# Performance work log

Hardware: AMD Instinct MI355X
Metric: run time of the kernel (lower is better)

## Reference

```python
import jax, jax.numpy as jnp
import numpy as np

N = 1_000_000   # active voxels
CIN = 32
COUT = 64
K = 9           # 3x3 kernel offsets (rulebook size)
EPS = 1e-5


def setup_inputs() -> dict:
    key = jax.random.key(0)
    ks = jax.random.split(key, 6)
    x = jax.random.normal(ks[0], (N, CIN), dtype=jnp.float32)
    # rulebook: neighbor index per (voxel, kernel offset); stride=1 so same coord set
    nbr = jax.random.randint(ks[1], (N, K), 0, N, dtype=jnp.int32)
    W1 = jax.random.normal(ks[2], (K, CIN, COUT), dtype=jnp.float32) * (1.0 / np.sqrt(K * CIN))
    W2 = jax.random.normal(ks[3], (K, COUT, COUT), dtype=jnp.float32) * (1.0 / np.sqrt(K * COUT))
    Wd = jax.random.normal(ks[4], (CIN, COUT), dtype=jnp.float32) * (1.0 / np.sqrt(CIN))
    g1 = jnp.ones((COUT,), jnp.float32); b1 = jnp.zeros((COUT,), jnp.float32)
    g2 = jnp.ones((COUT,), jnp.float32); b2 = jnp.zeros((COUT,), jnp.float32)
    gd = jnp.ones((COUT,), jnp.float32); bd = jnp.zeros((COUT,), jnp.float32)
    return {"x": x, "W1": W1, "g1": g1, "b1": b1, "W2": W2, "g2": g2, "b2": b2,
            "Wd": Wd, "gd": gd, "bd": bd, "nbr": nbr}


def _sparse_conv(x, nbr, W):
    # gather-GEMM-scatter; loop over the fixed K=9 kernel offsets to avoid
    # materializing the full [N, K, Cin] gathered tensor
    out = jnp.zeros((x.shape[0], W.shape[-1]), dtype=x.dtype)
    for k in range(W.shape[0]):
        out = out + jnp.take(x, nbr[:, k], axis=0) @ W[k]
    return out


def _bn(x, gamma, beta):
    # BatchNorm1d over the voxel dimension (training-mode batch statistics)
    mu = jnp.mean(x, axis=0)
    var = jnp.var(x, axis=0)
    return gamma * (x - mu) * jax.lax.rsqrt(var + EPS) + beta


def reference(x, W1, g1, b1, W2, g2, b2, Wd, gd, bd, nbr):
    # downsample branch (1x1 conv -> BN, no relu) since in_ch != out_ch
    identity = _bn(x @ Wd, gd, bd)
    # conv1: SparseConv3x3 -> BN -> ReLU
    out = jax.nn.relu(_bn(_sparse_conv(x, nbr, W1), g1, b1))
    # conv2: SparseConv3x3 -> BN (no relu)
    out = _bn(_sparse_conv(out, nbr, W2), g2, b2)
    # residual add + final ReLU
    return jax.nn.relu(out + identity)
```

## Files before the change

kernel.cpp:

```cpp
#include <hip/hip_runtime.h>
#include <hip/hip_bf16.h>

#define NV 1000000
#define CI 32
#define CO 64
#define KK 9
#define NG (NV / 16)
#define EPSV 1e-5f

typedef __bf16 bf16x8 __attribute__((ext_vector_type(8)));
typedef __bf16 bf16x4 __attribute__((ext_vector_type(4)));
typedef float  f32x4  __attribute__((ext_vector_type(4)));

__device__ __forceinline__ f32x4 mfma16(bf16x8 a, bf16x8 b, f32x4 c) {
    return __builtin_amdgcn_mfma_f32_16x16x32_bf16(a, b, c, 0, 0, 0);
}

__device__ __forceinline__ float xredseg(float v) {
    v += __shfl_xor(v, 16, 64);
    v += __shfl_xor(v, 32, 64);
    return v;
}

__global__ void k_prep_w(const float* __restrict__ W1, const float* __restrict__ W2,
                         const float* __restrict__ Wd,
                         __bf16* __restrict__ W1T, __bf16* __restrict__ W2T,
                         __bf16* __restrict__ WdT) {
    int i = blockIdx.x * blockDim.x + threadIdx.x;
    const int n1 = KK * CO * CI;
    const int n2 = KK * CO * CO;
    const int nd = CO * CI;
    if (i < n1) {
        int k = i / (CO * CI), r = i % (CO * CI), co = r / CI, ci = r % CI;
        W1T[i] = (__bf16)W1[(k * CI + ci) * CO + co];
    } else if (i < n1 + n2) {
        int j = i - n1;
        int k = j / (CO * CO), r = j % (CO * CO), co = r / CO, ci = r % CO;
        W2T[j] = (__bf16)W2[(k * CO + ci) * CO + co];
    } else if (i < n1 + n2 + nd) {
        int j = i - n1 - n2;
        int co = j / CI, ci = j % CI;
        WdT[j] = (__bf16)Wd[ci * CO + co];
    }
}

__global__ void k_prep_x(const float* __restrict__ x, __bf16* __restrict__ xb) {
    int i = blockIdx.x * blockDim.x + threadIdx.x;
    const float4* px = (const float4*)x + 2 * (size_t)i;
    float4 u = px[0], v = px[1];
    bf16x8 o;
    o[0] = (__bf16)u.x; o[1] = (__bf16)u.y; o[2] = (__bf16)u.z; o[3] = (__bf16)u.w;
    o[4] = (__bf16)v.x; o[5] = (__bf16)v.y; o[6] = (__bf16)v.z; o[7] = (__bf16)v.w;
    *((bf16x8*)xb + i) = o;
}

__global__ __launch_bounds__(256, 2) void k_conv1(
    const __bf16* __restrict__ xb, const int* __restrict__ nbr,
    const __bf16* __restrict__ W1T, const __bf16* __restrict__ WdT,
    __bf16* __restrict__ y1b, float* __restrict__ stats) {
    __shared__ __align__(16) char w1smem[KK * CO * CI * 2];
    __shared__ __align__(16) char ystage[4][2048];

    const int lane = threadIdx.x & 63;
    const int w    = threadIdx.x >> 6;
    const int r    = lane & 15;
    const int seg  = lane >> 4;
    const int sseg = seg ^ ((r >> 1) & 3);

#pragma unroll
    for (int j = 0; j < 9; j++) {
        int c    = j * 256 + threadIdx.x;
        int segc = c & 3;
        int rc   = (c >> 2) & 15;
        int csrc = (c & ~3) | (segc ^ ((rc >> 1) & 3));
        const __bf16* srcp = W1T + (size_t)csrc * 8;
        __builtin_amdgcn_global_load_lds(
            (const __attribute__((address_space(1))) void*)srcp,
            (__attribute__((address_space(3))) void*)(w1smem + j * 4096 + w * 1024),
            16, 0, 0);
    }
    __syncthreads();

    bf16x8 wd[4];
#pragma unroll
    for (int t = 0; t < 4; t++)
        wd[t] = *(const bf16x8*)(WdT + (size_t)(t * 16 + r) * CI + seg * 8);

    float ps1[4] = {0.f,0.f,0.f,0.f}, pq1[4] = {0.f,0.f,0.f,0.f};
    float psd[4] = {0.f,0.f,0.f,0.f}, pqd[4] = {0.f,0.f,0.f,0.f};

    const int slot   = blockIdx.x * 4 + w;
    const int stride = gridDim.x * 4;
    const f32x4 z = {0.f, 0.f, 0.f, 0.f};

    auto loadIdx = [&](int (&idx)[KK], int tile) {
        const int* nb = nbr + (size_t)(tile * 16 + r) * KK;
#pragma unroll
        for (int k = 0; k < KK; k++) idx[k] = nb[k];
    };
    auto gather9 = [&](bf16x8 (&g)[KK], const int (&idx)[KK]) {
#pragma unroll
        for (int k = 0; k < KK; k++)
            g[k] = *(const bf16x8*)(xb + (size_t)idx[k] * CI + seg * 8);
    };
    auto loadAd = [&](int tile) {
        return *(const bf16x8*)(xb + (size_t)(tile * 16 + r) * CI + seg * 8);
    };
    auto compute = [&](int tile, const bf16x8 (&g)[KK], bf16x8 ad) {
        int w1off = 0;
        asm volatile("" : "+v"(w1off));
        const __bf16* wb = (const __bf16*)w1smem + w1off;

        f32x4 acc[4]  = {z, z, z, z};
        f32x4 accd[4] = {z, z, z, z};
#pragma unroll
        for (int t = 0; t < 4; t++) accd[t] = mfma16(ad, wd[t], accd[t]);
#pragma unroll
        for (int k = 0; k < KK; k++) {
#pragma unroll
            for (int t = 0; t < 4; t++) {
                bf16x8 b = *(const bf16x8*)(wb + k * 2048 + t * 512 + r * 32 + sseg * 8);
                acc[t] = mfma16(g[k], b, acc[t]);
            }
        }

        const int vb = tile * 16;
        char* yst = ystage[w];
#pragma unroll
        for (int t = 0; t < 4; t++) {
#pragma unroll
            for (int rr = 0; rr < 4; rr++) {
                float val = acc[t][rr];
                ps1[t] += val; pq1[t] += val * val;
                float dv = accd[t][rr];
                psd[t] += dv; pqd[t] += dv * dv;
                int row = seg * 4 + rr;
                int byte = row * 128 + ((t * 32 + 2 * r) ^ ((row & 7) << 4));
                *(__bf16*)(yst + byte) = (__bf16)val;
            }
        }
#pragma unroll
        for (int q = 0; q < 2; q++) {
            int c    = lane * 2 + q;
            int row  = c >> 3;
            int part = c & 7;
            bf16x8 v = *(const bf16x8*)(yst + row * 128 + ((part ^ (row & 7)) << 4));
            __builtin_nontemporal_store(
                v, (bf16x8*)(y1b + (size_t)vb * CO + (size_t)c * 8));
        }
    };

    int idx0[KK], idx1[KK];
    bf16x8 g0[KK], g1[KK];
    bf16x8 ad0, ad1;

    int it = slot;
    loadIdx(idx0, it);
    gather9(g0, idx0); ad0 = loadAd(it);
    int itn = it + stride;
    bool have = (itn < NG);
    if (have) loadIdx(idx1, itn);

    while (true) {
        if (have) {
            gather9(g1, idx1); ad1 = loadAd(itn);
            int it2 = itn + stride;
            if (it2 < NG) loadIdx(idx0, it2);
        }
        compute(it, g0, ad0);
        if (!have) break;
        it = itn; itn = it + stride; have = (itn < NG);

        if (have) {
            gather9(g0, idx0); ad0 = loadAd(itn);
            int it2 = itn + stride;
            if (it2 < NG) loadIdx(idx1, it2);
        }
        compute(it, g1, ad1);
        if (!have) break;
        it = itn; itn = it + stride; have = (itn < NG);
    }

#pragma unroll
    for (int t = 0; t < 4; t++) {
        ps1[t] = xredseg(ps1[t]); pq1[t] = xredseg(pq1[t]);
        psd[t] = xredseg(psd[t]); pqd[t] = xredseg(pqd[t]);
    }
    if (lane < 16) {
#pragma unroll
        for (int t = 0; t < 4; t++) {
            atomicAdd(&stats[0 * 64 + t * 16 + lane], ps1[t]);
            atomicAdd(&stats[1 * 64 + t * 16 + lane], pq1[t]);
            atomicAdd(&stats[2 * 64 + t * 16 + lane], psd[t]);
            atomicAdd(&stats[3 * 64 + t * 16 + lane], pqd[t]);
        }
    }
}

#define TILE_B (16 * KK * 128)

template <bool BF16OUT>
__global__ __launch_bounds__(128, 2) void k_conv2(
    const __bf16* __restrict__ h1b, const int* __restrict__ nbr,
    const __bf16* __restrict__ W2T, const float* __restrict__ g1,
    const float* __restrict__ b1,
    __bf16* __restrict__ y2b, float* __restrict__ y2f,
    float* __restrict__ stats) {
    __shared__ __align__(16) char smem[2][TILE_B];
    __shared__ __align__(16) char ystage2[2][1024];

    const int lane = threadIdx.x & 63;
    const int w    = threadIdx.x >> 6;
    const int r    = lane & 15;
    const int seg  = lane >> 4;
    const int p    = lane & 7;

    bf16x8 w2[KK][2][2];
#pragma unroll
    for (int k = 0; k < KK; k++)
#pragma unroll
        for (int t2 = 0; t2 < 2; t2++)
#pragma unroll
            for (int s = 0; s < 2; s++) {
                int co = w * 32 + t2 * 16 + r;
                int ci = s * 32 + seg * 8;
                w2[k][t2][s] = *(const bf16x8*)(W2T + ((size_t)(k * CO + co)) * CO + ci);
            }

    float scP[8], shP[8];
#pragma unroll
    for (int j = 0; j < 8; j++) {
        int c0 = p * 8 + j;
        float mu  = stats[c0] * (1.0f / NV);
        float var = stats[64 + c0] * (1.0f / NV) - mu * mu;
        float s   = g1[c0] * rsqrtf(var + EPSV);
        scP[j] = s; shP[j] = b1[c0] - mu * s;
    }

    int ri[9], dstoff[9];
#pragma unroll
    for (int s = 0; s < 9; s++) {
        int c = w * 576 + s * 64 + lane;
        int rIdx = c >> 3;
        int i = (rIdx * 57) >> 9;
        ri[s] = rIdx;
        dstoff[s] = rIdx * 128 + ((p ^ (i & 7)) * 16);
    }

    auto loadIdx = [&](int (&ix)[9], int tile) {
        const int* nb = nbr + (size_t)tile * (16 * KK);
#pragma unroll
        for (int s = 0; s < 9; s++) ix[s] = nb[ri[s]];
    };
    auto loadDat = [&](f32x4 (&d)[9], const int (&ix)[9]) {
#pragma unroll
        for (int s = 0; s < 9; s++)
            d[s] = *(const f32x4*)(h1b + (size_t)ix[s] * CO + p * 8);
    };
    auto xform = [&](char* tb, const f32x4 (&d)[9]) {
#pragma unroll
        for (int s = 0; s < 9; s++) {
            union { f32x4 f; bf16x8 b; } u; u.f = d[s];
            bf16x8 o;
#pragma unroll
            for (int j = 0; j < 8; j++)
                o[j] = (__bf16)fmaxf((float)u.b[j] * scP[j] + shP[j], 0.f);
            *(bf16x8*)(tb + dstoff[s]) = o;
        }
    };

    float ps[2] = {0.f, 0.f}, pq[2] = {0.f, 0.f};
    const f32x4 z = {0.f, 0.f, 0.f, 0.f};
    const int sw = r & 7;
    const int G = gridDim.x;

    int idxN[9]; f32x4 dat[9];
    int it = blockIdx.x;
    loadIdx(idxN, it);
    loadDat(dat, idxN);
    { int t1 = it + G;     loadIdx(idxN, t1 < NG ? t1 : NG - 1); }
    xform(smem[0], dat);
    loadDat(dat, idxN);
    { int t2 = it + 2 * G; loadIdx(idxN, t2 < NG ? t2 : NG - 1); }
    __syncthreads();
    int cur = 0;

    for (; it < NG; it += G) {
        const __bf16* base = (const __bf16*)smem[cur];
        f32x4 acc[2] = {z, z};
#pragma unroll
        for (int k = 0; k < KK; k++) {
            const __bf16* rp = base + (size_t)(r * KK + k) * 64;
            bf16x8 a0 = *(const bf16x8*)(rp + ((seg ^ sw) * 8));
            bf16x8 a1 = *(const bf16x8*)(rp + (((4 + seg) ^ sw) * 8));
            acc[0] = mfma16(a0, w2[k][0][0], acc[0]);
            acc[0] = mfma16(a1, w2[k][0][1], acc[0]);
            acc[1] = mfma16(a0, w2[k][1][0], acc[1]);
            acc[1] = mfma16(a1, w2[k][1][1], acc[1]);
        }

        const int vb = it * 16;
        if constexpr (BF16OUT) {
            char* yst = ystage2[w];
#pragma unroll
            for (int t2 = 0; t2 < 2; t2++) {
#pragma unroll
                for (int rr = 0; rr < 4; rr++) {
                    float val = acc[t2][rr];
                    ps[t2] += val; pq[t2] += val * val;
                    int row = seg * 4 + rr;
                    int byte = row * 64 + ((t2 * 32 + 2 * r) ^ ((row >> 2) << 4));
                    *(__bf16*)(yst + byte) = (__bf16)val;
                }
            }
            {
                int row  = lane >> 2;
                int part = lane & 3;
                bf16x8 v = *(const bf16x8*)(yst + row * 64 + ((part ^ (row >> 2)) << 4));
                __builtin_nontemporal_store(
                    v, (bf16x8*)(y2b + (size_t)(vb + row) * CO + w * 32 + part * 8));
            }
        } else {
#pragma unroll
            for (int t2 = 0; t2 < 2; t2++) {
#pragma unroll
                for (int rr = 0; rr < 4; rr++) {
                    float val = acc[t2][rr];
                    int row = vb + seg * 4 + rr;
                    int c = w * 32 + t2 * 16 + r;
                    __builtin_nontemporal_store(val, &y2f[(size_t)row * CO + c]);
                    ps[t2] += val; pq[t2] += val * val;
                }
            }
        }

        int nx = it + G;
        if (nx < NG) {
            xform(smem[cur ^ 1], dat);
            loadDat(dat, idxN);
            { int t3 = it + 3 * G; loadIdx(idxN, t3 < NG ? t3 : NG - 1); }
            __syncthreads();
            cur ^= 1;
        }
    }

#pragma unroll
    for (int t2 = 0; t2 < 2; t2++) { ps[t2] = xredseg(ps[t2]); pq[t2] = xredseg(pq[t2]); }
    if (lane < 16) {
#pragma unroll
        for (int t2 = 0; t2 < 2; t2++) {
            atomicAdd(&stats[4 * 64 + w * 32 + t2 * 16 + lane], ps[t2]);
            atomicAdd(&stats[5 * 64 + w * 32 + t2 * 16 + lane], pq[t2]);
        }
    }
}

template <bool BF16IN>
__global__ __launch_bounds__(256, 2) void k_final(
    const __bf16* __restrict__ xb, const __bf16* __restrict__ WdT,
    const __bf16* __restrict__ y2b,
    float* __restrict__ out, const float* __restrict__ stats,
    const float* __restrict__ g2, const float* __restrict__ b2,
    const float* __restrict__ gd, const float* __restrict__ bd) {
    __shared__ float s2[CO], sh2[CO], sdv[CO], shd[CO];
    int t = threadIdx.x;
    if (t < CO) {
        float mu2  = stats[4 * 64 + t] * (1.0f / NV);
        float var2 = stats[5 * 64 + t] * (1.0f / NV) - mu2 * mu2;
        float s = g2[t] * rsqrtf(var2 + EPSV);
        s2[t] = s; sh2[t] = b2[t] - mu2 * s;
        float mud  = stats[2 * 64 + t] * (1.0f / NV);
        float vard = stats[3 * 64 + t] * (1.0f / NV) - mud * mud;
        float sd = gd[t] * rsqrtf(vard + EPSV);
        sdv[t] = sd; shd[t] = bd[t] - mud * sd;
    }
    __syncthreads();

    const int lane = threadIdx.x & 63;
    const int w    = threadIdx.x >> 6;
    const int r    = lane & 15;
    const int seg  = lane >> 4;

    bf16x8 wd[4];
#pragma unroll
    for (int t4 = 0; t4 < 4; t4++)
        wd[t4] = *(const bf16x8*)(WdT + (size_t)(t4 * 16 + r) * CI + seg * 8);

    const int slot = blockIdx.x * 4 + w;
    const int nslots = gridDim.x * 4;
    const f32x4 z = {0.f, 0.f, 0.f, 0.f};

    for (int gid = slot; gid < NG; gid += nslots) {
        const int vb = gid * 16;
        const int v  = vb + r;
        bf16x8 ad = *(const bf16x8*)(xb + (size_t)v * CI + seg * 8);
        f32x4 accd[4] = {z, z, z, z};
#pragma unroll
        for (int t4 = 0; t4 < 4; t4++) accd[t4] = mfma16(ad, wd[t4], accd[t4]);
#pragma unroll
        for (int t4 = 0; t4 < 4; t4++) {
#pragma unroll
            for (int rr = 0; rr < 4; rr++) {
                int row = vb + seg * 4 + rr;
                int c = t4 * 16 + r;
                size_t o = (size_t)row * CO + c;
                float y2v;
                if constexpr (BF16IN) y2v = (float)y2b[o];
                else                  y2v = out[o];
                float res = s2[c] * y2v + sh2[c] + sdv[c] * accd[t4][rr] + shd[c];
                __builtin_nontemporal_store(fmaxf(res, 0.f), &out[o]);
            }
        }
    }
}

extern "C" void kernel_launch(void* const* d_in, const int* in_sizes, int n_in,
                              void* d_out, int out_size, void* d_ws, size_t ws_size,
                              hipStream_t stream) {
    const float* x  = (const float*)d_in[0];
    const float* W1 = (const float*)d_in[1];
    const float* g1 = (const float*)d_in[2];
    const float* b1 = (const float*)d_in[3];
    const float* W2 = (const float*)d_in[4];
    const float* g2 = (const float*)d_in[5];
    const float* b2 = (const float*)d_in[6];
    const float* Wd = (const float*)d_in[7];
    const float* gd = (const float*)d_in[8];
    const float* bd = (const float*)d_in[9];
    const int*  nbr = (const int*)d_in[10];

    char* ws = (char*)d_ws;
    __bf16* xb  = (__bf16*)ws;
    __bf16* y1b = (__bf16*)(ws + 64000000);
    __bf16* W1T = (__bf16*)(ws + 192000000);
    __bf16* W2T = W1T + KK * CO * CI;
    __bf16* WdT = W2T + KK * CO * CO;
    float* stats = (float*)(ws + 192000000 + 2 * (KK*CO*CI + KK*CO*CO + CO*CI));
    size_t y2off = ((192000000 + 2 * (KK*CO*CI + KK*CO*CO + CO*CI) + 6*64*4) + 255) & ~(size_t)255;
    __bf16* y2b = (__bf16*)(ws + y2off);
    bool bf16y2 = (ws_size >= y2off + (size_t)NV * CO * 2 + 256);

    hipMemsetAsync(stats, 0, 6 * 64 * sizeof(float), stream);

    int nprep = KK*CO*CI + KK*CO*CO + CO*CI;
    k_prep_w<<<(nprep + 255) / 256, 256, 0, stream>>>(W1, W2, Wd, W1T, W2T, WdT);
    k_prep_x<<<(NV * CI / 8) / 256, 256, 0, stream>>>(x, xb);
    k_conv1<<<768, 256, 0, stream>>>(xb, nbr, W1T, WdT, y1b, stats);
    if (bf16y2) {
        k_conv2<true><<<1024, 128, 0, stream>>>(y1b, nbr, W2T, g1, b1,
                                                y2b, nullptr, stats);
        k_final<true><<<1024, 256, 0, stream>>>(xb, WdT, y2b, (float*)d_out, stats,
                                                g2, b2, gd, bd);
    } else {
        k_conv2<false><<<1024, 128, 0, stream>>>(y1b, nbr, W2T, g1, b1,
                                                 nullptr, (float*)d_out, stats);
        k_final<false><<<1024, 256, 0, stream>>>(xb, WdT, nullptr, (float*)d_out, stats,
                                                 g2, b2, gd, bd);
    }
}
```

Baseline: 591.3 us.

## Merge prep kernels and store conv1 output directly without LDS staging

Combines the weight-transpose and x-to-bf16 prep kernels into a single launch, removing one kernel launch. In conv1, the LDS transpose staging of the output tile is removed and each lane writes scalar bf16 values straight to global memory with nontemporal stores. This drops the shared-memory traffic and frees LDS, but replaces 16-byte coalesced stores with scattered 2-byte stores. That risks more memory transactions and lower write efficiency for the 128 MB y1 buffer.

```diff
diff --git a/kernel.cpp b/kernel.cpp
--- a/kernel.cpp
+++ b/kernel.cpp
@@ -22,36 +22,38 @@
     return v;
 }
 
-__global__ void k_prep_w(const float* __restrict__ W1, const float* __restrict__ W2,
-                         const float* __restrict__ Wd,
-                         __bf16* __restrict__ W1T, __bf16* __restrict__ W2T,
-                         __bf16* __restrict__ WdT) {
-    int i = blockIdx.x * blockDim.x + threadIdx.x;
-    const int n1 = KK * CO * CI;
-    const int n2 = KK * CO * CO;
-    const int nd = CO * CI;
-    if (i < n1) {
-        int k = i / (CO * CI), r = i % (CO * CI), co = r / CI, ci = r % CI;
-        W1T[i] = (__bf16)W1[(k * CI + ci) * CO + co];
-    } else if (i < n1 + n2) {
-        int j = i - n1;
-        int k = j / (CO * CO), r = j % (CO * CO), co = r / CO, ci = r % CO;
-        W2T[j] = (__bf16)W2[(k * CO + ci) * CO + co];
-    } else if (i < n1 + n2 + nd) {
-        int j = i - n1 - n2;
-        int co = j / CI, ci = j % CI;
-        WdT[j] = (__bf16)Wd[ci * CO + co];
-    }
-}
-
-__global__ void k_prep_x(const float* __restrict__ x, __bf16* __restrict__ xb) {
-    int i = blockIdx.x * blockDim.x + threadIdx.x;
-    const float4* px = (const float4*)x + 2 * (size_t)i;
-    float4 u = px[0], v = px[1];
-    bf16x8 o;
-    o[0] = (__bf16)u.x; o[1] = (__bf16)u.y; o[2] = (__bf16)u.z; o[3] = (__bf16)u.w;
-    o[4] = (__bf16)v.x; o[5] = (__bf16)v.y; o[6] = (__bf16)v.z; o[7] = (__bf16)v.w;
-    *((bf16x8*)xb + i) = o;
+__global__ void k_prep(const float* __restrict__ x, __bf16* __restrict__ xb,
+                       const float* __restrict__ W1, const float* __restrict__ W2,
+                       const float* __restrict__ Wd,
+                       __bf16* __restrict__ W1T, __bf16* __restrict__ W2T,
+                       __bf16* __restrict__ WdT) {
+    int bid = blockIdx.x;
+    if (bid < 15625) {
+        int i = bid * 256 + threadIdx.x;
+        const float4* px = (const float4*)x + 2 * (size_t)i;
+        float4 u = px[0], v = px[1];
+        bf16x8 o;
+        o[0] = (__bf16)u.x; o[1] = (__bf16)u.y; o[2] = (__bf16)u.z; o[3] = (__bf16)u.w;
+        o[4] = (__bf16)v.x; o[5] = (__bf16)v.y; o[6] = (__bf16)v.z; o[7] = (__bf16)v.w;
+        *((bf16x8*)xb + i) = o;
+    } else {
+        int i = (bid - 15625) * 256 + threadIdx.x;
+        const int n1 = KK * CO * CI;
+        const int n2 = KK * CO * CO;
+        const int nd = CO * CI;
+        if (i < n1) {
+            int k = i / (CO * CI), r = i % (CO * CI), co = r / CI, ci = r % CI;
+            W1T[i] = (__bf16)W1[(k * CI + ci) * CO + co];
+        } else if (i < n1 + n2) {
+            int j = i - n1;
+            int k = j / (CO * CO), r = j % (CO * CO), co = r / CO, ci = r % CO;
+            W2T[j] = (__bf16)W2[(k * CO + ci) * CO + co];
+        } else if (i < n1 + n2 + nd) {
+            int j = i - n1 - n2;
+            int co = j / CI, ci = j % CI;
+            WdT[j] = (__bf16)Wd[ci * CO + co];
+        }
+    }
 }
 
 __global__ __launch_bounds__(256, 2) void k_conv1(
@@ -59,7 +61,6 @@
     const __bf16* __restrict__ W1T, const __bf16* __restrict__ WdT,
     __bf16* __restrict__ y1b, float* __restrict__ stats) {
     __shared__ __align__(16) char w1smem[KK * CO * CI * 2];
-    __shared__ __align__(16) char ystage[4][2048];
 
     const int lane = threadIdx.x & 63;
     const int w    = threadIdx.x >> 6;
@@ -125,28 +126,17 @@
         }
 
         const int vb = tile * 16;
-        char* yst = ystage[w];
 #pragma unroll
         for (int t = 0; t < 4; t++) {
 #pragma unroll
             for (int rr = 0; rr < 4; rr++) {
                 float val = acc[t][rr];
+                int row = vb + seg * 4 + rr;
+                __builtin_nontemporal_store((__bf16)val, &y1b[(size_t)row * CO + t * 16 + r]);
                 ps1[t] += val; pq1[t] += val * val;
                 float dv = accd[t][rr];
                 psd[t] += dv; pqd[t] += dv * dv;
-                int row = seg * 4 + rr;
-                int byte = row * 128 + ((t * 32 + 2 * r) ^ ((row & 7) << 4));
-                *(__bf16*)(yst + byte) = (__bf16)val;
-            }
-        }
-#pragma unroll
-        for (int q = 0; q < 2; q++) {
-            int c    = lane * 2 + q;
-            int row  = c >> 3;
-            int part = c & 7;
-            bf16x8 v = *(const bf16x8*)(yst + row * 128 + ((part ^ (row & 7)) << 4));
-            __builtin_nontemporal_store(
-                v, (bf16x8*)(y1b + (size_t)vb * CO + (size_t)c * 8));
+            }
         }
     };
 
@@ -442,9 +432,7 @@
 
     hipMemsetAsync(stats, 0, 6 * 64 * sizeof(float), stream);
 
-    int nprep = KK*CO*CI + KK*CO*CO + CO*CI;
-    k_prep_w<<<(nprep + 255) / 256, 256, 0, stream>>>(W1, W2, Wd, W1T, W2T, WdT);
-    k_prep_x<<<(NV * CI / 8) / 256, 256, 0, stream>>>(x, xb);
+    k_prep<<<15625 + 224, 256, 0, stream>>>(x, xb, W1, W2, Wd, W1T, W2T, WdT);
     k_conv1<<<768, 256, 0, stream>>>(xb, nbr, W1T, WdT, y1b, stats);
     if (bf16y2) {
         k_conv2<true><<<1024, 128, 0, stream>>>(y1b, nbr, W2T, g1, b1,
```

Result: faster. 577.8 us (-2.3%).
